# Performance work log

Measured on AMD Instinct MI355X. Metric: run time of the kernel, lower is better.

Reference implementation:

```python
import jax, jax.numpy as jnp
import numpy as np

B, N, H = 16, 1024, 768
NEG_INF = -9e15
SLOPE = 0.2


def setup_inputs() -> dict:
    key = jax.random.key(0)
    k1, k2, k3, k4, k5 = jax.random.split(key, 5)
    x = jax.random.normal(k1, (B, N, H), dtype=jnp.float32)
    # node_length acts as a per-node validity mask (float, used via outer product)
    lengths = jax.random.randint(k2, (B,), N // 2, N)
    node_length = (jnp.arange(N)[None, :] < lengths[:, None]).astype(jnp.float32)
    # sparse-ish binary adjacency with self-loops
    adj = (jax.random.uniform(k3, (B, N, N)) < 0.05).astype(jnp.float32)
    adj = jnp.maximum(adj, jnp.eye(N, dtype=jnp.float32)[None])
    # params: kaiming-normal init
    W = jax.random.normal(k4, (H, H), dtype=jnp.float32) * np.sqrt(2.0 / H)
    a = jax.random.normal(k5, (2 * H, 1), dtype=jnp.float32) * np.sqrt(2.0 / (2 * H))
    return {"input": x, "node_length": node_length, "graph_structure": adj, "W": W, "a": a}


def reference(input, node_length, graph_structure, W, a):
    # node_vec = A @ X  [B,N,H]
    node_vec = jnp.matmul(graph_structure, input)
    h = jnp.matmul(node_vec, W)  # [B,N,F]
    F_ = W.shape[1]
    a1 = a[:F_, 0]   # weights on h_i
    a2 = a[F_:, 0]   # weights on h_j
    # e[b,i,j] = leaky_relu(h_i . a1 + h_j . a2)  (identical to concat+matmul with a)
    s1 = jnp.einsum("bnf,f->bn", h, a1)
    s2 = jnp.einsum("bnf,f->bn", h, a2)
    e = jax.nn.leaky_relu(s1[:, :, None] + s2[:, None, :], negative_slope=SLOPE)
    # bias = outer product of node_length; mask where adj or bias <= 1e-6
    bias = node_length[:, :, None] * node_length[:, None, :]
    valid = (graph_structure > 1e-6) & (bias > 1e-6)
    scores = jnp.where(valid, e, NEG_INF)
    attn = jax.nn.softmax(scores, axis=-1)  # attn_dropout=0 -> identity
    return node_vec, attn
```

## Files before the change

kernel.cpp:

```cpp
#include <hip/hip_runtime.h>
#include <hip/hip_bf16.h>

#define BB 16
#define NN 1024
#define HH 768
#define NEG_INF_ -9.0e15f
#define SLOPE_ 0.2f

typedef __bf16 bh8 __attribute__((ext_vector_type(8)));
typedef __bf16 bh4 __attribute__((ext_vector_type(4)));
typedef float f4 __attribute__((ext_vector_type(4)));
typedef unsigned int u32;
typedef unsigned long long u64;


__device__ __forceinline__ float wave_sum0(float v) {
    #pragma unroll
    for (int off = 32; off > 0; off >>= 1) v += __shfl_down(v, off, 64);
    return v;
}
__device__ __forceinline__ float wave_sum_all(float v) {
    #pragma unroll
    for (int off = 1; off < 64; off <<= 1) v += __shfl_xor(v, off, 64);
    return v;
}
__device__ __forceinline__ float wave_max_all(float v) {
    #pragma unroll
    for (int off = 1; off < 64; off <<= 1) v = fmaxf(v, __shfl_xor(v, off, 64));
    return v;
}


__device__ __forceinline__ void gl_lds16(const void* g, void* l) {
    __builtin_amdgcn_global_load_lds(
        (const __attribute__((address_space(1))) u32*)g,
        (__attribute__((address_space(3))) u32*)l, 16, 0, 0);
}


__global__ __launch_bounds__(256) void prep_xt_kernel(const float* __restrict__ adj,
                                                      const float* __restrict__ W,
                                                      const float* __restrict__ a,
                                                      const float* __restrict__ x,
                                                      u64* __restrict__ bits,
                                                      __bf16* __restrict__ xT,
                                                      float* __restrict__ wa1,
                                                      float* __restrict__ wa2,
                                                      float* __restrict__ s1,
                                                      float* __restrict__ s2) {
    __shared__ __bf16 T[32][36];
    const int bid = blockIdx.x;
    const int tid = threadIdx.x;
    const int wave = tid >> 6, lane = tid & 63;

    if (bid < 4096) {
        const int gid = bid * 256 + tid;
        if (gid < BB * NN) { s1[gid] = 0.f; s2[gid] = 0.f; }

        const int row = bid * 4 + wave;
        const float* ar = adj + (size_t)row * NN;
        const int seg = lane >> 4;
        const int sh = (lane & 15) * 4;
        #pragma unroll
        for (int i = 0; i < 4; i++) {
            const int j = lane * 4 + i * 256;
            const f4 av = __builtin_nontemporal_load((const f4*)(ar + j));
            u32 nib = (av[0] > 1e-6f ? 1u : 0u) | (av[1] > 1e-6f ? 2u : 0u)
                    | (av[2] > 1e-6f ? 4u : 0u) | (av[3] > 1e-6f ? 8u : 0u);
            u64 word = (u64)nib << sh;
            word |= __shfl_xor(word, 8, 16);
            word |= __shfl_xor(word, 4, 16);
            word |= __shfl_xor(word, 2, 16);
            word |= __shfl_xor(word, 1, 16);
            if ((lane & 15) == 0) bits[(size_t)row * 16 + i * 4 + seg] = word;
        }

        if (bid < 192) {
            const int f = bid * 4 + wave;
            const float* Wr = W + (size_t)f * HH;
            float v1 = 0.f, v2 = 0.f;
            #pragma unroll
            for (int i = 0; i < 3; i++) {
                const int h = lane * 4 + i * 256;
                const float4 w  = *(const float4*)(Wr + h);
                const float4 a1 = *(const float4*)(a + h);
                const float4 a2 = *(const float4*)(a + HH + h);
                v1 += w.x * a1.x + w.y * a1.y + w.z * a1.z + w.w * a1.w;
                v2 += w.x * a2.x + w.y * a2.y + w.z * a2.z + w.w * a2.w;
            }
            v1 = wave_sum0(v1);
            v2 = wave_sum0(v2);
            if (lane == 0) { wa1[f] = v1; wa2[f] = v2; }
        }
    } else {
        const int u = bid - 4096;
        const int ht = u % 24;
        const int nt = (u / 24) & 31;
        const int b  = u / (24 * 32);
        const int r = tid >> 3;
        const int c = (tid & 7) * 4;
        const float4 v = *(const float4*)(x + ((size_t)b * NN + nt * 32 + r) * HH + ht * 32 + c);
        T[r][c + 0] = (__bf16)v.x; T[r][c + 1] = (__bf16)v.y;
        T[r][c + 2] = (__bf16)v.z; T[r][c + 3] = (__bf16)v.w;

        __syncthreads();
        const int h = tid >> 3;
        const int nc = (tid & 7) * 4;
        bh4 o = { T[nc + 0][h], T[nc + 1][h], T[nc + 2][h], T[nc + 3][h] };
        *(bh4*)(xT + ((size_t)b * HH + ht * 32 + h) * NN + nt * 32 + nc) = o;
    }
}


#define BW 17

__global__ __launch_bounds__(256) void gemm_bits(const u64* __restrict__ bits,
                                                 const __bf16* __restrict__ xT,
                                                 const float* __restrict__ wa1,
                                                 const float* __restrict__ wa2,
                                                 float* __restrict__ out,
                                                 float* __restrict__ s1,
                                                 float* __restrict__ s2) {
    __shared__ __bf16 LUT[256 * 8];
    __shared__ u64 bitsL[128 * BW];
    __shared__ __bf16 Bs[2][128 * 64];

    const int orig = blockIdx.x;
    const int g  = (orig >> 6) * 8 + (orig & 7);
    const int bm = (orig >> 3) & 7;
    const int b  = g / 6;
    const int bn = g % 6;

    const int tid = threadIdx.x, lane = tid & 63, wave = tid >> 6;
    const int wr = (wave >> 1) << 6;
    const int wc = (wave & 1) << 6;
    const int quad = lane >> 4, l16 = lane & 15;

    {
        bh8 e;
        #pragma unroll
        for (int j = 0; j < 8; j++) e[j] = ((tid >> j) & 1) ? (__bf16)1.0f : (__bf16)0.0f;
        *(bh8*)&LUT[tid * 8] = e;
    }
    {
        const u64* bg = bits + ((size_t)b * NN + bm * 128) * 16;
        #pragma unroll
        for (int q = 0; q < 8; q++) {
            const int gw = tid * 8 + q;
            bitsL[(gw >> 4) * BW + (gw & 15)] = bg[gw];
        }
    }

    const __bf16* Xb = xT + ((size_t)b * HH + bn * 128) * NN;

    const __bf16* sSrc[4]; int sOff[4];
    #pragma unroll
    for (int it = 0; it < 4; it++) {
        const int c = tid + 256 * it;
        const int r = c >> 3, j = c & 7, kc = j ^ (r & 7);
        sSrc[it] = Xb + (size_t)r * NN + kc * 8;
        sOff[it] = c * 8;
    }

    f4 acc[4][4];
    #pragma unroll
    for (int i = 0; i < 4; i++)
        #pragma unroll
        for (int j = 0; j < 4; j++)
            acc[i][j] = (f4){0.f, 0.f, 0.f, 0.f};

    #pragma unroll
    for (int it = 0; it < 4; it++) gl_lds16(sSrc[it] + 0,  &Bs[0][sOff[it]]);
    #pragma unroll
    for (int it = 0; it < 4; it++) gl_lds16(sSrc[it] + 64, &Bs[1][sOff[it]]);
    asm volatile("s_waitcnt lgkmcnt(0) vmcnt(4)" ::: "memory");
    __builtin_amdgcn_s_barrier();
    asm volatile("" ::: "memory");

    for (int w = 0; w < 16; ++w) {
        const int cur = w & 1;

        u64 aw[4];
        #pragma unroll
        for (int i = 0; i < 4; i++)
            aw[i] = bitsL[(wr + i * 16 + l16) * BW + w];

        __builtin_amdgcn_s_setprio(1);
        #pragma unroll
        for (int s = 0; s < 2; s++) {
            bh8 af[4], bf_[4];
            #pragma unroll
            for (int i = 0; i < 4; i++) {
                const u32 byte = (u32)(aw[i] >> ((s * 4 + quad) * 8)) & 0xffu;
                af[i] = *(const bh8*)&LUT[byte * 8];
            }
            #pragma unroll
            for (int j = 0; j < 4; j++) {
                const int row = wc + j * 16 + l16;
                const int jj = (s * 4 + quad) ^ (row & 7);
                bf_[j] = *(const bh8*)&Bs[cur][row * 64 + jj * 8];
            }
            #pragma unroll
            for (int i = 0; i < 4; i++)
                #pragma unroll
                for (int j = 0; j < 4; j++)
                    acc[i][j] = __builtin_amdgcn_mfma_f32_16x16x32_bf16(af[i], bf_[j], acc[i][j], 0, 0, 0);
        }
        __builtin_amdgcn_s_setprio(0);

        if (w < 14) {
            __builtin_amdgcn_s_barrier();
            asm volatile("" ::: "memory");
            const int kt = (w + 2) << 6;
            #pragma unroll
            for (int it = 0; it < 4; it++) gl_lds16(sSrc[it] + kt, &Bs[cur][sOff[it]]);
            asm volatile("s_waitcnt vmcnt(4)" ::: "memory");
            __builtin_amdgcn_s_barrier();
            asm volatile("" ::: "memory");
        } else if (w == 14) {
            asm volatile("s_waitcnt vmcnt(0)" ::: "memory");
            __builtin_amdgcn_s_barrier();
            asm volatile("" ::: "memory");
        }
    }

    float* Cb = out + (size_t)b * NN * HH + (size_t)bm * 128 * HH + bn * 128;
    const int rbase = wr + quad * 4;
    const int cbase = wc + l16;
    #pragma unroll
    for (int i = 0; i < 4; i++)
        #pragma unroll
        for (int j = 0; j < 4; j++)
            #pragma unroll
            for (int r = 0; r < 4; r++)
                __builtin_nontemporal_store(acc[i][j][r],
                    &Cb[(size_t)(rbase + i * 16 + r) * HH + cbase + j * 16]);

    float w1j[4], w2j[4];
    #pragma unroll
    for (int j = 0; j < 4; j++) {
        w1j[j] = wa1[bn * 128 + cbase + j * 16];
        w2j[j] = wa2[bn * 128 + cbase + j * 16];
    }
    #pragma unroll
    for (int i = 0; i < 4; i++)
        #pragma unroll
        for (int r = 0; r < 4; r++) {
            float p1 = acc[i][0][r] * w1j[0] + acc[i][1][r] * w1j[1]
                     + acc[i][2][r] * w1j[2] + acc[i][3][r] * w1j[3];
            float p2 = acc[i][0][r] * w2j[0] + acc[i][1][r] * w2j[1]
                     + acc[i][2][r] * w2j[2] + acc[i][3][r] * w2j[3];
            p1 += __shfl_down(p1, 8, 16); p1 += __shfl_down(p1, 4, 16);
            p1 += __shfl_down(p1, 2, 16); p1 += __shfl_down(p1, 1, 16);
            p2 += __shfl_down(p2, 8, 16); p2 += __shfl_down(p2, 4, 16);
            p2 += __shfl_down(p2, 2, 16); p2 += __shfl_down(p2, 1, 16);
            if (l16 == 0) {
                const int n = b * NN + bm * 128 + rbase + i * 16 + r;
                atomicAdd(&s1[n], p1);
                atomicAdd(&s2[n], p2);
            }
        }
}


__global__ __launch_bounds__(256) void softmax_kernel(const u64* __restrict__ bits,
                                                      const float* __restrict__ nl,
                                                      const float* __restrict__ s1,
                                                      const float* __restrict__ s2,
                                                      float* __restrict__ attn) {
    const int row = blockIdx.x * 4 + (threadIdx.x >> 6);
    const int lane = threadIdx.x & 63;
    const int b = row >> 10, n = row & (NN - 1);
    const u64* bwr = bits + (size_t)row * 16;
    const float* nlb = nl + (size_t)b * NN;
    const float* s2b = s2 + (size_t)b * NN;
    const float s1v = s1[row];
    const bool rowok = nlb[n] > 1e-6f;
    const int bitbase = (lane & 15) * 4;

    f4 sc[4];
    float mx = NEG_INF_;
    #pragma unroll
    for (int i = 0; i < 4; i++) {
        const int j = lane * 4 + i * 256;
        const float4 sv = *(const float4*)(s2b + j);
        const float4 nv = *(const float4*)(nlb + j);
        const u64 w64 = bwr[i * 4 + (lane >> 4)];
        const float zs[4] = { s1v + sv.x, s1v + sv.y, s1v + sv.z, s1v + sv.w };
        const float ns[4] = { nv.x, nv.y, nv.z, nv.w };
        #pragma unroll
        for (int e = 0; e < 4; e++) {
            const float z = zs[e];
            const float lr = z > 0.f ? z : SLOPE_ * z;
            const bool valid = rowok && ((w64 >> (bitbase + e)) & 1ull) && (ns[e] > 1e-6f);
            sc[i][e] = valid ? lr : NEG_INF_;
            mx = fmaxf(mx, sc[i][e]);
        }
    }
    mx = wave_max_all(mx);

    f4 ex[4];
    float sum = 0.f;
    #pragma unroll
    for (int i = 0; i < 4; i++)
        #pragma unroll
        for (int e = 0; e < 4; e++) {
            ex[i][e] = __expf(sc[i][e] - mx);
            sum += ex[i][e];
        }
    sum = wave_sum_all(sum);
    const float inv = 1.0f / sum;

    float* outr = attn + (size_t)row * NN;
    #pragma unroll
    for (int i = 0; i < 4; i++) {
        const int j = lane * 4 + i * 256;
        f4 o;
        o[0] = ex[i][0] * inv; o[1] = ex[i][1] * inv;
        o[2] = ex[i][2] * inv; o[3] = ex[i][3] * inv;
        __builtin_nontemporal_store(o, (f4*)(outr + j));
    }
}


extern "C" void kernel_launch(void* const* d_in, const int* in_sizes, int n_in,
                              void* d_out, int out_size, void* d_ws, size_t ws_size,
                              hipStream_t stream) {
    const float* x   = (const float*)d_in[0];
    const float* nl  = (const float*)d_in[1];
    const float* adj = (const float*)d_in[2];
    const float* W   = (const float*)d_in[3];
    const float* a   = (const float*)d_in[4];

    float* out = (float*)d_out;
    float* node_vec = out;
    float* attn = out + (size_t)BB * NN * HH;

    char* wsb = (char*)d_ws;
    float* wa1 = (float*)(wsb);
    float* wa2 = wa1 + HH;
    float* s1  = wa2 + HH;
    float* s2  = s1 + BB * NN;
    u64*    bits = (u64*)(wsb + (1u << 20));
    __bf16* xT   = (__bf16*)(wsb + (4u << 20));

    hipLaunchKernelGGL(prep_xt_kernel, dim3(4096 + 24 * 32 * BB), dim3(256), 0, stream,
                       adj, W, a, x, bits, xT, wa1, wa2, s1, s2);
    hipLaunchKernelGGL(gemm_bits, dim3(768), dim3(256), 0, stream,
                       bits, xT, wa1, wa2, node_vec, s1, s2);
    hipLaunchKernelGGL(softmax_kernel, dim3(4096), dim3(256), 0, stream, bits, nl, s1, s2, attn);
}
```

Measured before the change: 259.5 us.

## Load GEMM B fragments directly from global memory instead of LDS double buffer

Removes the LDS double-buffered staging of the xT tile (global_load_lds with swizzle and per-iteration barriers) and has each lane read its bf16 B fragments straight from global memory into registers. This drops the barriers and LDS traffic and frees shared memory, which may allow higher occupancy. The trade-off is that the two waves sharing a column tile now fetch the same B data separately, and there is no explicit prefetch, so global load latency is exposed inside the k-loop unless the compiler or other waves hide it.

```diff
diff --git a/kernel.cpp b/kernel.cpp
--- a/kernel.cpp
+++ b/kernel.cpp
@@ -28,13 +28,6 @@
     #pragma unroll
     for (int off = 1; off < 64; off <<= 1) v = fmaxf(v, __shfl_xor(v, off, 64));
     return v;
-}
-
-
-__device__ __forceinline__ void gl_lds16(const void* g, void* l) {
-    __builtin_amdgcn_global_load_lds(
-        (const __attribute__((address_space(1))) u32*)g,
-        (__attribute__((address_space(3))) u32*)l, 16, 0, 0);
 }
 
 
@@ -123,7 +116,6 @@
                                                  float* __restrict__ s2) {
     __shared__ __bf16 LUT[256 * 8];
     __shared__ u64 bitsL[128 * BW];
-    __shared__ __bf16 Bs[2][128 * 64];
 
     const int orig = blockIdx.x;
     const int g  = (orig >> 6) * 8 + (orig & 7);
@@ -153,14 +145,10 @@
 
     const __bf16* Xb = xT + ((size_t)b * HH + bn * 128) * NN;
 
-    const __bf16* sSrc[4]; int sOff[4];
-    #pragma unroll
-    for (int it = 0; it < 4; it++) {
-        const int c = tid + 256 * it;
-        const int r = c >> 3, j = c & 7, kc = j ^ (r & 7);
-        sSrc[it] = Xb + (size_t)r * NN + kc * 8;
-        sOff[it] = c * 8;
-    }
+    const __bf16* bRow[4];
+    #pragma unroll
+    for (int j = 0; j < 4; j++)
+        bRow[j] = Xb + (size_t)(wc + j * 16 + l16) * NN + quad * 8;
 
     f4 acc[4][4];
     #pragma unroll
@@ -169,59 +157,37 @@
         for (int j = 0; j < 4; j++)
             acc[i][j] = (f4){0.f, 0.f, 0.f, 0.f};
 
-    #pragma unroll
-    for (int it = 0; it < 4; it++) gl_lds16(sSrc[it] + 0,  &Bs[0][sOff[it]]);
-    #pragma unroll
-    for (int it = 0; it < 4; it++) gl_lds16(sSrc[it] + 64, &Bs[1][sOff[it]]);
-    asm volatile("s_waitcnt lgkmcnt(0) vmcnt(4)" ::: "memory");
-    __builtin_amdgcn_s_barrier();
-    asm volatile("" ::: "memory");
+    __syncthreads();
 
     for (int w = 0; w < 16; ++w) {
-        const int cur = w & 1;
-
         u64 aw[4];
         #pragma unroll
         for (int i = 0; i < 4; i++)
             aw[i] = bitsL[(wr + i * 16 + l16) * BW + w];
 
+        bh8 bf_[2][4];
+        #pragma unroll
+        for (int s = 0; s < 2; s++)
+            #pragma unroll
+            for (int j = 0; j < 4; j++)
+                bf_[s][j] = *(const bh8*)(bRow[j] + w * 64 + s * 32);
+
         __builtin_amdgcn_s_setprio(1);
         #pragma unroll
         for (int s = 0; s < 2; s++) {
-            bh8 af[4], bf_[4];
+            bh8 af[4];
             #pragma unroll
             for (int i = 0; i < 4; i++) {
                 const u32 byte = (u32)(aw[i] >> ((s * 4 + quad) * 8)) & 0xffu;
                 af[i] = *(const bh8*)&LUT[byte * 8];
             }
             #pragma unroll
-            for (int j = 0; j < 4; j++) {
-                const int row = wc + j * 16 + l16;
-                const int jj = (s * 4 + quad) ^ (row & 7);
-                bf_[j] = *(const bh8*)&Bs[cur][row * 64 + jj * 8];
-            }
-            #pragma unroll
             for (int i = 0; i < 4; i++)
                 #pragma unroll
                 for (int j = 0; j < 4; j++)
-                    acc[i][j] = __builtin_amdgcn_mfma_f32_16x16x32_bf16(af[i], bf_[j], acc[i][j], 0, 0, 0);
+                    acc[i][j] = __builtin_amdgcn_mfma_f32_16x16x32_bf16(af[i], bf_[s][j], acc[i][j], 0, 0, 0);
         }
         __builtin_amdgcn_s_setprio(0);
-
-        if (w < 14) {
-            __builtin_amdgcn_s_barrier();
-            asm volatile("" ::: "memory");
-            const int kt = (w + 2) << 6;
-            #pragma unroll
-            for (int it = 0; it < 4; it++) gl_lds16(sSrc[it] + kt, &Bs[cur][sOff[it]]);
-            asm volatile("s_waitcnt vmcnt(4)" ::: "memory");
-            __builtin_amdgcn_s_barrier();
-            asm volatile("" ::: "memory");
-        } else if (w == 14) {
-            asm volatile("s_waitcnt vmcnt(0)" ::: "memory");
-            __builtin_amdgcn_s_barrier();
-            asm volatile("" ::: "memory");
-        }
     }
 
     float* Cb = out + (size_t)b * NN * HH + (size_t)bm * 128 * HH + bn * 128;
```

Result: slower. 267.7 us (+3.1%).
